# Kernel optimization log

Measured on AMD Instinct MI355X. Metric: run time of the kernel, lower is better.

Reference implementation:

```python
import jax, jax.numpy as jnp
import numpy as np

NUM_EMBEDDINGS = 1024
EMBEDDING_DIM = 256


def setup_inputs() -> dict:
    key = jax.random.key(0)
    kx, kw = jax.random.split(key)
    x = jax.random.normal(kx, (64, 32, 32, EMBEDDING_DIM), dtype=jnp.float32)
    # nn.Embedding default init: N(0, 1)
    embedding_weight = jax.random.normal(kw, (NUM_EMBEDDINGS, EMBEDDING_DIM), dtype=jnp.float32)
    return {"x": x, "embedding_weight": embedding_weight}


def reference(x, embedding_weight):
    D = embedding_weight.shape[1]
    x_flat = x.reshape(-1, D)  # [N, D]
    distances = (
        jnp.sum(x_flat * x_flat, axis=1, keepdims=True)
        + jnp.sum(embedding_weight * embedding_weight, axis=1)
        - 2.0 * jnp.matmul(x_flat, embedding_weight.T)
    )
    indices = jnp.argmin(distances, axis=1)  # [N]
    quantized = embedding_weight[indices].reshape(x.shape)
    return quantized, indices
```

## Files before the change

### kernel.cpp

```cpp
#include <hip/hip_runtime.h>


#define K_EMB  1024
#define D_DIM  256
#define N_ROWS 65536

typedef unsigned int u32;
typedef unsigned long long u64;
typedef __attribute__((ext_vector_type(8)))  _Float16 f16x8;
typedef __attribute__((ext_vector_type(4)))  _Float16 f16x4;
typedef __attribute__((ext_vector_type(16))) float    f32x16;

#define GLDS(gp, lp) __builtin_amdgcn_global_load_lds( \
    (const __attribute__((address_space(1))) void*)(gp), \
    (__attribute__((address_space(3))) void*)(lp), 16, 0, 0)

__global__ void vq_prep(const float* __restrict__ emb,
                        _Float16* __restrict__ ehi,
                        u32* __restrict__ cn2c,
                        float* __restrict__ cnormf) {
    int gid = blockIdx.x * 256 + threadIdx.x;
    int code = gid >> 6, lane = gid & 63;
    float4 v = ((const float4*)(emb + (size_t)code * D_DIM))[lane];
    f16x4 hv = {(_Float16)v.x, (_Float16)v.y, (_Float16)v.z, (_Float16)v.w};
    ((f16x4*)(ehi + (size_t)code * D_DIM))[lane] = hv;
    float s = v.x * v.x + v.y * v.y + v.z * v.z + v.w * v.w;
    #pragma unroll
    for (int off = 32; off > 0; off >>= 1) s += __shfl_down(s, off, 64);
    if (lane == 0) {
        float cn = 0.5f * s;
        cnormf[code] = cn;
        _Float16 ch = (_Float16)cn;
        _Float16 cl = (_Float16)(cn - (float)ch);
        union { _Float16 hh[2]; u32 uu; } pk;
        pk.hh[0] = (_Float16)(-(float)ch);
        pk.hh[1] = (_Float16)(-(float)cl);
        cn2c[code] = pk.uu;
    }
}

__global__ __launch_bounds__(512, 4) void vq_main(
    const float* __restrict__ x, const float* __restrict__ emb,
    const _Float16* __restrict__ eh, const u32* __restrict__ cn2c,
    const float* __restrict__ cnormf,
    float* __restrict__ outq, float* __restrict__ outi)
{
    __shared__ _Float16 T[2][2][8192];
    __shared__ u32 CNs[1024];
    __shared__ u32 xchg[2][128][3];
    __shared__ int winners[128];

    const int t = threadIdx.x, w = t >> 6, lane = t & 63;
    const int m = lane & 31, kh = lane >> 5;
    const int p = w >> 1;
    const int h = w & 1;
    const int blkrow = blockIdx.x * 128;
    const int kh4 = kh * 4;
    const float NEGINF = __uint_as_float(0xFF800000u);

    auto stage = [&](int c) {
        _Float16* dstb = &T[c & 1][h][0];
        const _Float16* srcb = eh + (size_t)(h * 512 + c * 32 + m) * D_DIM + kh * 8;
        #pragma unroll
        for (int i = 0; i < 4; i++) {
            int r = p * 4 + i;
            GLDS(srcb + r * 16, dstb + r * 512);
        }
    };

    stage(0);

    CNs[t] = cn2c[t];
    CNs[t + 512] = cn2c[t + 512];

    f16x8 bh[16];
    {
        char* xb = (char*)&T[1][0][0];
        #pragma unroll
        for (int k = 0; k < 2; k++) {
            #pragma unroll
            for (int i = 0; i < 8; i++) {
                int row = i * 8 + w;
                float4 v = *(const float4*)(
                    x + (size_t)(blkrow + k * 64 + row) * D_DIM + lane * 4);
                f16x4 hv = {(_Float16)v.x, (_Float16)v.y,
                            (_Float16)v.z, (_Float16)v.w};
                u32 byte = (u32)(row * 512 + lane * 8) ^ ((u32)(row & 7) << 4);
                *(f16x4*)(xb + byte) = hv;
            }
            __syncthreads();
            if ((p >> 1) == k) {
                int lr = (p & 1) * 32 + m;
                #pragma unroll
                for (int s = 0; s < 16; s++) {
                    u32 byte = (u32)(lr * 512 + s * 32 + kh * 16)
                             ^ ((u32)(lr & 7) << 4);
                    bh[s] = *(const f16x8*)(xb + byte);
                }
            }
            __syncthreads();
        }
    }
    f16x8 xe = {};
    if (kh == 0) { xe[0] = (_Float16)1.0f; xe[1] = (_Float16)1.0f; }

    float B1 = NEGINF, B2 = NEGINF, B3 = NEGINF;

    auto t3f = [](float& c1, float& c2, float& c3, float pv) {
        float n3 = __builtin_amdgcn_fmed3f(c2, pv, c3);
        float n2 = __builtin_amdgcn_fmed3f(c1, pv, c2);
        c1 = fmaxf(c1, pv);
        c2 = n2; c3 = n3;
    };

    auto computeMF = [&](int buf, f32x16& a, int c) {
        const f16x8* Af = (const f16x8*)&T[buf][h][0];
        union { u32 uu; _Float16 hh[2]; } uv;
        uv.uu = CNs[h * 512 + c * 32 + m];
        f16x8 e = {};
        e[0] = uv.hh[0]; e[1] = uv.hh[1];
        a = (f32x16){};
        __builtin_amdgcn_s_setprio(1);
        #pragma unroll
        for (int s = 0; s < 16; s++) {
            f16x8 fa = Af[(2 * s + kh) * 32 + m];
            a = __builtin_amdgcn_mfma_f32_32x32x16_f16(fa, bh[s], a, 0, 0, 0);
        }
        a = __builtin_amdgcn_mfma_f32_32x32x16_f16(e, xe, a, 0, 0, 0);
        __builtin_amdgcn_s_setprio(0);
    };

    auto top3p = [&](const f32x16& a, int c) {
        const u32 sbase = (u32)(h * 512 + c * 32) + kh4;
        #pragma unroll
        for (int r = 0; r < 16; r++) {
            u32 code = sbase + (r & 3) + 8 * (r >> 2);
            u32 bits = (__float_as_uint(a[r]) & 0xFFFFFC00u) | code;
            t3f(B1, B2, B3, __uint_as_float(bits));
        }
    };

    f32x16 accA, accB;
    for (int cc = 0; cc < 16; cc += 2) {
        __builtin_amdgcn_sched_barrier(0);
        __builtin_amdgcn_s_barrier();
        stage(cc + 1);
        asm volatile("s_waitcnt vmcnt(4)" ::: "memory");
        __builtin_amdgcn_sched_barrier(0);
        __builtin_amdgcn_s_barrier();
        computeMF(0, accA, cc);
        if (cc) top3p(accB, cc - 1);

        __builtin_amdgcn_sched_barrier(0);
        __builtin_amdgcn_s_barrier();
        if (cc + 2 < 16) {
            stage(cc + 2);
            asm volatile("s_waitcnt vmcnt(4)" ::: "memory");
        } else {
            asm volatile("s_waitcnt vmcnt(0)" ::: "memory");
        }
        __builtin_amdgcn_sched_barrier(0);
        __builtin_amdgcn_s_barrier();
        computeMF(1, accB, cc + 1);
        top3p(accA, cc);
    }
    top3p(accB, 15);

    {
        float q1 = __shfl_xor(B1, 32, 64);
        float q2 = __shfl_xor(B2, 32, 64);
        float q3 = __shfl_xor(B3, 32, 64);
        t3f(B1, B2, B3, q1); t3f(B1, B2, B3, q2); t3f(B1, B2, B3, q3);
    }

    if (kh == 0) {
        int ra = p * 32 + m;
        xchg[h][ra][0] = __float_as_uint(B1);
        xchg[h][ra][1] = __float_as_uint(B2);
        xchg[h][ra][2] = __float_as_uint(B3);
    }
    __syncthreads();

    const int lr = w * 16 + (lane & 15);
    float c1 = NEGINF, c2 = NEGINF, c3 = NEGINF;
    #pragma unroll
    for (int hh = 0; hh < 2; hh++) {
        t3f(c1, c2, c3, __uint_as_float(xchg[hh][lr][0]));
        t3f(c1, c2, c3, __uint_as_float(xchg[hh][lr][1]));
        t3f(c1, c2, c3, __uint_as_float(xchg[hh][lr][2]));
    }

    u32 i1 = __float_as_uint(c1) & 1023u;
    u32 i2 = __float_as_uint(c2) & 1023u;
    u32 i3 = __float_as_uint(c3) & 1023u;
    const bool act = lane < 16;
    bool need = (c1 - c2) <= 0.25f;
    if (act && !need) winners[lr] = (int)i1;
    u64 mask = __ballot(act && need);
    while (mask) {
        int r = __ffsll((unsigned long long)mask) - 1;
        mask &= mask - 1;
        int row = blkrow + w * 16 + r;
        u32 d1 = (u32)__shfl((int)i1, r, 64);
        u32 d2 = (u32)__shfl((int)i2, r, 64);
        u32 d3 = (u32)__shfl((int)i3, r, 64);
        float g3 = __shfl(c1 - c3, r, 64);
        int ncand = (g3 <= 0.25f) ? 3 : 2;
        float4 xv = ((const float4*)(x + (size_t)row * D_DIM))[lane];
        float bs = -3.0e38f; int bi = 0x7fffffff;
        u32 cand[3] = {d1, d2, d3};
        for (int q = 0; q < ncand; q++) {
            int ccd = (int)cand[q];
            float4 ev = ((const float4*)(emb + (size_t)ccd * D_DIM))[lane];
            float d = xv.x * ev.x + xv.y * ev.y + xv.z * ev.z + xv.w * ev.w;
            #pragma unroll
            for (int dd = 1; dd < 64; dd <<= 1) d += __shfl_xor(d, dd, 64);
            float sc = d - cnormf[ccd];
            if (sc > bs || (sc == bs && ccd < bi)) { bs = sc; bi = ccd; }
        }
        if (lane == 0) winners[w * 16 + r] = bi;
    }

    if (act) outi[blkrow + lr] = (float)winners[lr];
    #pragma unroll 8
    for (int r = 0; r < 16; r++) {
        int idx = winners[w * 16 + r];
        int row = blkrow + w * 16 + r;
        float4 qv = ((const float4*)(emb + (size_t)idx * D_DIM))[lane];
        ((float4*)(outq + (size_t)row * D_DIM))[lane] = qv;
    }
}

extern "C" void kernel_launch(void* const* d_in, const int* in_sizes, int n_in,
                              void* d_out, int out_size, void* d_ws, size_t ws_size,
                              hipStream_t stream) {
    const float* x   = (const float*)d_in[0];
    const float* emb = (const float*)d_in[1];
    float* outq = (float*)d_out;
    float* outi = outq + (size_t)N_ROWS * D_DIM;

    _Float16* ehi = (_Float16*)d_ws;
    u32* cn2c = (u32*)(ehi + (size_t)K_EMB * D_DIM);
    float* cnormf = (float*)(cn2c + K_EMB);

    vq_prep<<<K_EMB / 4, 256, 0, stream>>>(emb, ehi, cn2c, cnormf);
    vq_main<<<N_ROWS / 128, 512, 0, stream>>>(x, emb, ehi, cn2c, cnormf,
                                              outq, outi);
}
```

Baseline: 160.3 us.

## Replace two-buffer ping-pong loop with single-barrier loop and split MFMA accumulators

The main distance loop drops the manually interleaved schedule, which overlapped each chunk's top-3 selection with the next chunk's MFMA. It becomes one iteration per chunk with a single barrier, and the next chunk's prefetch is issued right after that barrier. The 16-step MFMA reduction is split into two independent accumulator chains (low and high halves of D) that are summed before top-3 selection, to shorten the dependent MFMA chain. In exchange, this wave no longer overlaps its own top-3 VALU work with MFMA and relies on other resident waves to hide it. Summing two partial accumulators can also change fp32 rounding slightly.

```diff
diff --git a/kernel.cpp b/kernel.cpp
--- a/kernel.cpp
+++ b/kernel.cpp
@@ -113,58 +113,40 @@
         c2 = n2; c3 = n3;
     };
 
-    auto computeMF = [&](int buf, f32x16& a, int c) {
-        const f16x8* Af = (const f16x8*)&T[buf][h][0];
+    for (int c = 0; c < 16; ++c) {
+        asm volatile("s_waitcnt vmcnt(0)" ::: "memory");
+        __builtin_amdgcn_sched_barrier(0);
+        __builtin_amdgcn_s_barrier();
+        __builtin_amdgcn_sched_barrier(0);
+        if (c + 1 < 16) stage(c + 1);
+
+        const f16x8* Af = (const f16x8*)&T[c & 1][h][0];
         union { u32 uu; _Float16 hh[2]; } uv;
         uv.uu = CNs[h * 512 + c * 32 + m];
         f16x8 e = {};
         e[0] = uv.hh[0]; e[1] = uv.hh[1];
-        a = (f32x16){};
+
+        f32x16 alo = {}, ahi = {};
         __builtin_amdgcn_s_setprio(1);
         #pragma unroll
-        for (int s = 0; s < 16; s++) {
-            f16x8 fa = Af[(2 * s + kh) * 32 + m];
-            a = __builtin_amdgcn_mfma_f32_32x32x16_f16(fa, bh[s], a, 0, 0, 0);
-        }
-        a = __builtin_amdgcn_mfma_f32_32x32x16_f16(e, xe, a, 0, 0, 0);
+        for (int s = 0; s < 8; s++) {
+            f16x8 fl = Af[(2 * s + kh) * 32 + m];
+            f16x8 fh = Af[(2 * (s + 8) + kh) * 32 + m];
+            alo = __builtin_amdgcn_mfma_f32_32x32x16_f16(fl, bh[s],     alo, 0, 0, 0);
+            ahi = __builtin_amdgcn_mfma_f32_32x32x16_f16(fh, bh[s + 8], ahi, 0, 0, 0);
+        }
+        ahi = __builtin_amdgcn_mfma_f32_32x32x16_f16(e, xe, ahi, 0, 0, 0);
         __builtin_amdgcn_s_setprio(0);
-    };
-
-    auto top3p = [&](const f32x16& a, int c) {
+
         const u32 sbase = (u32)(h * 512 + c * 32) + kh4;
         #pragma unroll
         for (int r = 0; r < 16; r++) {
             u32 code = sbase + (r & 3) + 8 * (r >> 2);
-            u32 bits = (__float_as_uint(a[r]) & 0xFFFFFC00u) | code;
+            float sc = alo[r] + ahi[r];
+            u32 bits = (__float_as_uint(sc) & 0xFFFFFC00u) | code;
             t3f(B1, B2, B3, __uint_as_float(bits));
         }
-    };
-
-    f32x16 accA, accB;
-    for (int cc = 0; cc < 16; cc += 2) {
-        __builtin_amdgcn_sched_barrier(0);
-        __builtin_amdgcn_s_barrier();
-        stage(cc + 1);
-        asm volatile("s_waitcnt vmcnt(4)" ::: "memory");
-        __builtin_amdgcn_sched_barrier(0);
-        __builtin_amdgcn_s_barrier();
-        computeMF(0, accA, cc);
-        if (cc) top3p(accB, cc - 1);
-
-        __builtin_amdgcn_sched_barrier(0);
-        __builtin_amdgcn_s_barrier();
-        if (cc + 2 < 16) {
-            stage(cc + 2);
-            asm volatile("s_waitcnt vmcnt(4)" ::: "memory");
-        } else {
-            asm volatile("s_waitcnt vmcnt(0)" ::: "memory");
-        }
-        __builtin_amdgcn_sched_barrier(0);
-        __builtin_amdgcn_s_barrier();
-        computeMF(1, accB, cc + 1);
-        top3p(accA, cc);
-    }
-    top3p(accB, 15);
+    }
 
     {
         float q1 = __shfl_xor(B1, 32, 64);
```

Result: slower. 192.1 us (+19.8%).
